# Performance work log

Hardware: AMD Instinct MI355X
Metric: run time of the kernel (lower is better)

## Reference

```python
import jax, jax.numpy as jnp
import numpy as np

NUM_CAPS = 32
OUT_DIM = 8   # capsule vector length in channel terms; note the view() below mixes spatial dims
H_OUT = 6
W_OUT = 6


def setup_inputs() -> dict:
    key = jax.random.key(0)
    k1, k2, k3 = jax.random.split(key, 3)
    X = jax.random.normal(k1, (512, 256, 20, 20), dtype=jnp.float32)
    # 32 Conv2d(256->8, k=9) stacked capsule-major into one grouped-output conv
    W = jax.random.normal(k2, (256, 256, 9, 9), dtype=jnp.float32) * 0.02
    b = jax.random.normal(k3, (256,), dtype=jnp.float32) * 0.02
    return {"X": X, "W": W, "b": b}


def squash(u):
    # u: [B, 1152, 8]; squash along last dim (matches torch code exactly)
    ns = jnp.sum(u * u, axis=-1, keepdims=True)
    return ns / (1.0 + ns) * (u / (0.001 + jnp.sqrt(ns)))


def reference(X, W, b):
    # One conv replaces the 32 separate Conv2d modules; output channels are
    # ordered [cap0_ch0..cap0_ch7, cap1_ch0..], identical to torch.stack(dim=1)
    # followed by contiguous view.
    y = jax.lax.conv_general_dilated(
        X, W, window_strides=(2, 2), padding='VALID',
        dimension_numbers=('NCHW', 'OIHW', 'NCHW'))  # [B, 256, 6, 6]
    y = y + b[None, :, None, None]
    B = X.shape[0]
    # torch: stack -> [B,32,8,6,6] -> view(B, 32*36, -1) is a raw contiguous
    # reshape; [B,256,6,6] has the same memory layout, so reshape directly.
    u = y.reshape(B, NUM_CAPS * H_OUT * W_OUT, OUT_DIM)  # [B, 1152, 8]
    return squash(u)
```

## Files before the change

### kernel.cpp

```cpp
#include <hip/hip_runtime.h>
#include <hip/hip_bf16.h>
#include <stdint.h>

typedef __attribute__((ext_vector_type(8))) short bf16x8;
typedef __attribute__((ext_vector_type(4))) float f32x4;

__device__ __forceinline__ unsigned short f2bf(float f) {
  union { float f; unsigned int u; } v; v.f = f;
  unsigned int u = v.u;
  u += 0x7fffu + ((u >> 16) & 1u);
  return (unsigned short)(u >> 16);
}

__global__ __launch_bounds__(256) void xform_x(const float* __restrict__ X,
                                               unsigned short* __restrict__ Xt) {
  const int b = blockIdx.x;
  const int t = threadIdx.x;
  const float* src = X + ((size_t)b * 256 + t) * 400;
  unsigned short* dst = Xt + (size_t)b * 400 * 256 + t;
  for (int hw = 0; hw < 400; hw += 4) {
    float4 v = *(const float4*)(src + hw);
    dst[(size_t)(hw + 0) * 256] = f2bf(v.x);
    dst[(size_t)(hw + 1) * 256] = f2bf(v.y);
    dst[(size_t)(hw + 2) * 256] = f2bf(v.z);
    dst[(size_t)(hw + 3) * 256] = f2bf(v.w);
  }
}

__global__ __launch_bounds__(256) void xform_w(const float* __restrict__ W,
                                               unsigned short* __restrict__ Wt) {
  __shared__ unsigned short lds[81 * 128];
  const int co = blockIdx.x;
  const int ct = blockIdx.y;
  const int t = threadIdx.x;
  const float* src = W + ((size_t)co * 256 + (size_t)ct * 128) * 81;
  for (int idx = t; idx < 128 * 81; idx += 256) {
    int ci_l = idx / 81, khw = idx - ci_l * 81;
    lds[khw * 128 + ci_l] = f2bf(src[idx]);
  }
  __syncthreads();
  unsigned short* dst = Wt + (size_t)co * 256 + (size_t)ct * 128;
  for (int idx = t; idx < 81 * 128; idx += 256) {
    int khw = idx >> 7, ci_l = idx & 127;
    dst[(size_t)khw * 65536 + ci_l] = lds[idx];
  }
}

__device__ __forceinline__ void gload16(const unsigned short* g, unsigned short* l) {
  __builtin_amdgcn_global_load_lds(
      (const __attribute__((address_space(1))) unsigned int*)g,
      (__attribute__((address_space(3))) unsigned int*)l, 16, 0, 0);
}

__global__ __launch_bounds__(256, 3) void conv_gemm(
    const unsigned short* __restrict__ Xt,
    const unsigned short* __restrict__ Wt,
    const float* __restrict__ bias,
    float* __restrict__ Y) {
  __shared__ __align__(16) unsigned short lds[20480];
  const int mt = blockIdx.x;
  const int nt = blockIdx.y;
  const int t = threadIdx.x;
  const int c16 = t & 15, rq = t >> 4;
  const int swz = (c16 ^ (rq & 7)) * 8;

  int xb[6];
  #pragma unroll
  for (int r = 0; r < 6; ++r) {
    int m = mt * 96 + r * 16 + rq;
    int b = m / 36, s = m - b * 36;
    int oh = s / 6, ow = s - oh * 6;
    xb[r] = ((b * 20 + 2 * oh) * 20 + 2 * ow) * 256 + swz;
  }
  int wb[4];
  #pragma unroll
  for (int r = 0; r < 4; ++r) wb[r] = (nt * 64 + r * 16 + rq) * 256 + swz;

  const int dA = t * 8;
  const int dB = 12288 + t * 8;

  const int lane = t & 63, wv = t >> 6;
  const int wm = (wv >> 1) * 48, wn = (wv & 1) * 32;
  const int l15 = lane & 15, l4 = lane >> 4, l7s = lane & 7;

  int aOff[3][4], bOff[2][4];
  #pragma unroll
  for (int i = 0; i < 3; ++i)
    #pragma unroll
    for (int kk = 0; kk < 4; ++kk)
      aOff[i][kk] = (wm + i * 16 + l15) * 128 +
                    (((kk * 4 + l4) ^ (l15 & 7)) * 8);
  #pragma unroll
  for (int j = 0; j < 2; ++j)
    #pragma unroll
    for (int kk = 0; kk < 4; ++kk)
      bOff[j][kk] = 12288 + (wn + j * 16 + l15) * 128 +
                    (((kk * 4 + l4) ^ (l15 & 7)) * 8);

  f32x4 acc[3][2];
  #pragma unroll
  for (int i = 0; i < 3; ++i)
    #pragma unroll
    for (int j = 0; j < 2; ++j) acc[i][j] = (f32x4){0.f, 0.f, 0.f, 0.f};

  int s_ci = 0, s_kw = 0, xo = 0, wo = 0;
  auto adv = [&]() {
    if (s_ci == 0) { s_ci = 1; xo += 128; wo += 128; }
    else {
      s_ci = 0; wo += 65536 - 128;
      if (s_kw < 8) { ++s_kw; xo += 128; }
      else          { s_kw = 0; xo += 2944; }
    }
  };
  auto stage = [&]() {
    #pragma unroll
    for (int r = 0; r < 6; ++r) gload16(Xt + xb[r] + xo, lds + dA + r * 2048);
    #pragma unroll
    for (int r = 0; r < 4; ++r) gload16(Wt + wb[r] + wo, lds + dB + r * 2048);
  };
  auto compute = [&]() {
    bf16x8 af[3][4], bfr[2][4];
    #pragma unroll
    for (int i = 0; i < 3; ++i)
      #pragma unroll
      for (int kk = 0; kk < 4; ++kk) af[i][kk] = *(const bf16x8*)(lds + aOff[i][kk]);
    #pragma unroll
    for (int j = 0; j < 2; ++j)
      #pragma unroll
      for (int kk = 0; kk < 4; ++kk) bfr[j][kk] = *(const bf16x8*)(lds + bOff[j][kk]);
    #pragma unroll
    for (int kk = 0; kk < 4; ++kk)
      #pragma unroll
      for (int i = 0; i < 3; ++i)
        #pragma unroll
        for (int j = 0; j < 2; ++j)
          acc[i][j] = __builtin_amdgcn_mfma_f32_16x16x32_bf16(
              af[i][kk], bfr[j][kk], acc[i][j], 0, 0, 0);
  };

  #pragma unroll 1
  for (int s = 0; s < 162; ++s) {
    stage(); adv();
    __syncthreads();
    compute();
    __syncthreads();
  }

  #pragma unroll
  for (int j = 0; j < 2; ++j) {
    int co = nt * 64 + wn + j * 16 + l15;
    float bb = bias[co];
    #pragma unroll
    for (int i = 0; i < 3; ++i) {
      int m0 = mt * 96 + wm + i * 16 + l4 * 4;
      #pragma unroll
      for (int q = 0; q < 4; ++q) {
        int m = m0 + q;
        int b = m / 36, s = m - b * 36;
        Y[((size_t)b * 256 + co) * 36 + s] = acc[i][j][q] + bb;
      }
    }
  }
}

__global__ __launch_bounds__(256) void squash_k(float* __restrict__ Y) {
  const int g = blockIdx.x * 256 + threadIdx.x;
  float4* p = (float4*)(Y + (size_t)g * 8);
  float4 a = p[0], b = p[1];
  float ns = a.x * a.x + a.y * a.y + a.z * a.z + a.w * a.w +
             b.x * b.x + b.y * b.y + b.z * b.z + b.w * b.w;
  float sc = ns / ((1.0f + ns) * (0.001f + sqrtf(ns)));
  a.x *= sc; a.y *= sc; a.z *= sc; a.w *= sc;
  b.x *= sc; b.y *= sc; b.z *= sc; b.w *= sc;
  p[0] = a; p[1] = b;
}

extern "C" void kernel_launch(void* const* d_in, const int* in_sizes, int n_in,
                              void* d_out, int out_size, void* d_ws, size_t ws_size,
                              hipStream_t stream) {
  const float* X = (const float*)d_in[0];
  const float* W = (const float*)d_in[1];
  const float* bias = (const float*)d_in[2];
  float* Y = (float*)d_out;

  unsigned short* Xt = (unsigned short*)d_ws;
  unsigned short* Wt = Xt + (size_t)512 * 400 * 256;

  xform_x<<<512, 256, 0, stream>>>(X, Xt);
  xform_w<<<dim3(256, 2), 256, 0, stream>>>(W, Wt);
  conv_gemm<<<dim3(192, 4), 256, 0, stream>>>(Xt, Wt, bias, Y);
  squash_k<<<2304, 256, 0, stream>>>(Y);
}
```

Measured before the change: 407.5 us.

## Split LDS K-tile into two 64-wide halves and swizzle block order

```diff
diff --git a/kernel.cpp b/kernel.cpp
--- a/kernel.cpp
+++ b/kernel.cpp
@@ -58,44 +58,47 @@
     const float* __restrict__ bias,
     float* __restrict__ Y) {
   __shared__ __align__(16) unsigned short lds[20480];
-  const int mt = blockIdx.x;
-  const int nt = blockIdx.y;
+  const int flat = blockIdx.x + gridDim.x * blockIdx.y;
+  const int swzb = (flat & 7) * 96 + (flat >> 3);
+  const int mt = swzb % 192;
+  const int nt = swzb / 192;
   const int t = threadIdx.x;
-  const int c16 = t & 15, rq = t >> 4;
-  const int swz = (c16 ^ (rq & 7)) * 8;
-
-  int xb[6];
-  #pragma unroll
-  for (int r = 0; r < 6; ++r) {
-    int m = mt * 96 + r * 16 + rq;
+  const int c8 = t & 7, rq = t >> 3;
+  const int swz = (c8 ^ (rq & 7)) * 8;
+
+  int xb[3];
+  #pragma unroll
+  for (int r = 0; r < 3; ++r) {
+    int m = mt * 96 + r * 32 + rq;
     int b = m / 36, s = m - b * 36;
     int oh = s / 6, ow = s - oh * 6;
     xb[r] = ((b * 20 + 2 * oh) * 20 + 2 * ow) * 256 + swz;
   }
-  int wb[4];
-  #pragma unroll
-  for (int r = 0; r < 4; ++r) wb[r] = (nt * 64 + r * 16 + rq) * 256 + swz;
-
-  const int dA = t * 8;
-  const int dB = 12288 + t * 8;
+  int wb[2];
+  #pragma unroll
+  for (int r = 0; r < 2; ++r) wb[r] = (nt * 64 + r * 32 + rq) * 256 + swz;
 
   const int lane = t & 63, wv = t >> 6;
   const int wm = (wv >> 1) * 48, wn = (wv & 1) * 32;
-  const int l15 = lane & 15, l4 = lane >> 4, l7s = lane & 7;
-
-  int aOff[3][4], bOff[2][4];
+  const int l15 = lane & 15, l4 = lane >> 4, l7 = l15 & 7;
+
+  int aOff[3][2][2], bOff[2][2][2];
   #pragma unroll
   for (int i = 0; i < 3; ++i)
     #pragma unroll
-    for (int kk = 0; kk < 4; ++kk)
-      aOff[i][kk] = (wm + i * 16 + l15) * 128 +
-                    (((kk * 4 + l4) ^ (l15 & 7)) * 8);
+    for (int h = 0; h < 2; ++h)
+      #pragma unroll
+      for (int kk = 0; kk < 2; ++kk)
+        aOff[i][h][kk] = h * 6144 + (wm + i * 16 + l15) * 64 +
+                         (((kk * 4 + l4) ^ l7) * 8);
   #pragma unroll
   for (int j = 0; j < 2; ++j)
     #pragma unroll
-    for (int kk = 0; kk < 4; ++kk)
-      bOff[j][kk] = 12288 + (wn + j * 16 + l15) * 128 +
-                    (((kk * 4 + l4) ^ (l15 & 7)) * 8);
+    for (int h = 0; h < 2; ++h)
+      #pragma unroll
+      for (int kk = 0; kk < 2; ++kk)
+        bOff[j][h][kk] = 12288 + h * 4096 + (wn + j * 16 + l15) * 64 +
+                         (((kk * 4 + l4) ^ l7) * 8);
 
   f32x4 acc[3][2];
   #pragma unroll
@@ -114,28 +117,42 @@
   };
   auto stage = [&]() {
     #pragma unroll
-    for (int r = 0; r < 6; ++r) gload16(Xt + xb[r] + xo, lds + dA + r * 2048);
-    #pragma unroll
-    for (int r = 0; r < 4; ++r) gload16(Wt + wb[r] + wo, lds + dB + r * 2048);
+    for (int r = 0; r < 3; ++r)
+      #pragma unroll
+      for (int h = 0; h < 2; ++h)
+        gload16(Xt + xb[r] + h * 64 + xo, lds + h * 6144 + t * 8 + r * 2048);
+    #pragma unroll
+    for (int r = 0; r < 2; ++r)
+      #pragma unroll
+      for (int h = 0; h < 2; ++h)
+        gload16(Wt + wb[r] + h * 64 + wo, lds + 12288 + h * 4096 + t * 8 + r * 2048);
   };
   auto compute = [&]() {
-    bf16x8 af[3][4], bfr[2][4];
+    bf16x8 af[3][2][2], bf[2][2][2];
     #pragma unroll
     for (int i = 0; i < 3; ++i)
       #pragma unroll
-      for (int kk = 0; kk < 4; ++kk) af[i][kk] = *(const bf16x8*)(lds + aOff[i][kk]);
+      for (int h = 0; h < 2; ++h)
+        #pragma unroll
+        for (int kk = 0; kk < 2; ++kk)
+          af[i][h][kk] = *(const bf16x8*)(lds + aOff[i][h][kk]);
     #pragma unroll
     for (int j = 0; j < 2; ++j)
       #pragma unroll
-      for (int kk = 0; kk < 4; ++kk) bfr[j][kk] = *(const bf16x8*)(lds + bOff[j][kk]);
-    #pragma unroll
-    for (int kk = 0; kk < 4; ++kk)
-      #pragma unroll
-      for (int i = 0; i < 3; ++i)
+      for (int h = 0; h < 2; ++h)
         #pragma unroll
-        for (int j = 0; j < 2; ++j)
-          acc[i][j] = __builtin_amdgcn_mfma_f32_16x16x32_bf16(
-              af[i][kk], bfr[j][kk], acc[i][j], 0, 0, 0);
+        for (int kk = 0; kk < 2; ++kk)
+          bf[j][h][kk] = *(const bf16x8*)(lds + bOff[j][h][kk]);
+    #pragma unroll
+    for (int h = 0; h < 2; ++h)
+      #pragma unroll
+      for (int kk = 0; kk < 2; ++kk)
+        #pragma unroll
+        for (int i = 0; i < 3; ++i)
+          #pragma unroll
+          for (int j = 0; j < 2; ++j)
+            acc[i][j] = __builtin_amdgcn_mfma_f32_16x16x32_bf16(
+                af[i][h][kk], bf[j][h][kk], acc[i][j], 0, 0, 0);
   };
 
   #pragma unroll 1
```

Result: slower. 549.6 us (+34.9%).
